# Kernel tuning notes

Hardware: AMD Instinct MI355X
Metric: run time of the kernel (lower is better)

## Reference

```python
import jax, jax.numpy as jnp
import numpy as np

NUM_EDGE_TYPES = 4
TIME_STEPS = (1, 1)  # one propagation step per layer, 2 layers
HIDDEN = 128
N_NODES = 50000
N_EDGES = 400000


def setup_inputs() -> dict:
    key = jax.random.key(0)
    ks = jax.random.split(key, 8)
    states = jax.random.normal(ks[0], (N_NODES, HIDDEN), jnp.float32)
    etype = jax.random.randint(ks[1], (N_EDGES,), 0, NUM_EDGE_TYPES, jnp.int32)
    src = jax.random.randint(ks[2], (N_EDGES,), 0, N_NODES, jnp.int32)
    dst = jax.random.randint(ks[3], (N_EDGES,), 0, N_NODES, jnp.int32)
    edges = jnp.stack([etype, src, dst], axis=-1)  # [E, 3] = (type, src, dst)
    L = len(TIME_STEPS)
    std = HIDDEN ** -0.5  # matches tf.random_normal_initializer(stddev=H**-0.5)
    type_W = jax.random.normal(ks[4], (L, NUM_EDGE_TYPES, HIDDEN, HIDDEN), jnp.float32) * std
    type_b = jax.random.normal(ks[5], (L, NUM_EDGE_TYPES, HIDDEN), jnp.float32) * std
    gru_kernel = jax.random.normal(ks[6], (L, HIDDEN, 3 * HIDDEN), jnp.float32) * std
    gru_rkernel = jax.random.normal(ks[7], (L, HIDDEN, 3 * HIDDEN), jnp.float32) * std
    gru_bias = jnp.zeros((L, 2, 3 * HIDDEN), jnp.float32)  # [input_bias, recurrent_bias]
    return dict(states=states, edges=edges, type_W=type_W, type_b=type_b,
                gru_kernel=gru_kernel, gru_rkernel=gru_rkernel, gru_bias=gru_bias)


def _gru_cell(x, h, kernel, rkernel, bias):
    # tf.keras.layers.GRUCell with defaults (reset_after=True, sigmoid/tanh)
    mx = x @ kernel + bias[0]   # [N, 3H]
    mh = h @ rkernel + bias[1]  # [N, 3H]
    xz, xr, xh = jnp.split(mx, 3, axis=-1)
    hz, hr, hh = jnp.split(mh, 3, axis=-1)
    z = jax.nn.sigmoid(xz + hz)
    r = jax.nn.sigmoid(xr + hr)
    c = jnp.tanh(xh + r * hh)
    return z * h + (1.0 - z) * c


def _propagate(h, layer_no, edges, type_W, type_b):
    etype, src, dst = edges[:, 0], edges[:, 1], edges[:, 2]
    src_states = h[src]  # [E, H] irregular gather
    msgs = jnp.zeros_like(src_states)
    # per-edge-type dense transform, combined via masking (jit-friendly
    # equivalent of tf.dynamic_partition + per-type matmul)
    for t in range(NUM_EDGE_TYPES):
        mt = src_states @ type_W[layer_no, t] + type_b[layer_no, t]
        msgs = msgs + jnp.where((etype == t)[:, None], mt, 0.0)
    # scatter-add messages into destination nodes
    return jax.ops.segment_sum(msgs, dst, num_segments=h.shape[0])


def reference(states, edges, type_W, type_b, gru_kernel, gru_rkernel, gru_bias):
    h = states
    for layer_no, steps in enumerate(TIME_STEPS):
        for _ in range(steps):
            agg = _propagate(h, layer_no, edges, type_W, type_b)
            h = _gru_cell(agg, h, gru_kernel[layer_no], gru_rkernel[layer_no], gru_bias[layer_no])
    return h
```

## Files before the change

### kernel.cpp

```cpp
#include <hip/hip_runtime.h>
#include <hip/hip_bf16.h>

#define H 128
#define NT 4
#define CAP4 40
#define BK 64

typedef __attribute__((ext_vector_type(8))) _Float16 half8;
typedef __attribute__((ext_vector_type(4))) float f32x4;

#if defined(__has_builtin)
#if __has_builtin(__builtin_amdgcn_global_load_lds)
#define HAS_GLL 1
#endif
#endif
#ifndef HAS_GLL
#define HAS_GLL 0
#endif

__device__ __forceinline__ float bf2f(unsigned short u) {
    union { unsigned int i; float f; } v;
    v.i = ((unsigned int)u) << 16;
    return v.f;
}

__device__ __forceinline__ unsigned short f2bf(float f) {
    union { float f; unsigned int i; } v;
    v.f = f;
    unsigned int x = v.i;
    unsigned int r = (x + 0x7fffu + ((x >> 16) & 1u)) >> 16;
    return (unsigned short)r;
}

__device__ __forceinline__ float fsigmoid(float x) {
    return 1.0f / (1.0f + __expf(-x));
}
__device__ __forceinline__ float ftanh(float x) {
    return 1.0f - 2.0f / (__expf(2.0f * x) + 1.0f);
}

__device__ __forceinline__ float readf(const void* p, long i, int isbf) {
    return isbf ? bf2f(((const unsigned short*)p)[i]) : ((const float*)p)[i];
}

__device__ __forceinline__ void gll16(const _Float16* g, _Float16* l) {
#if HAS_GLL
    __builtin_amdgcn_global_load_lds(
        (const __attribute__((address_space(1))) unsigned int*)g,
        (__attribute__((address_space(3))) unsigned int*)l, 16, 0, 0);
#endif
}

__device__ __forceinline__ void stage_tile(
    const _Float16* __restrict__ gbase, int rstride, int row0, int kof,
    int maxrow, _Float16* lds) {
    const int wave = threadIdx.x >> 6, lane = threadIdx.x & 63;
#pragma unroll
    for (int s = 0; s < 4; s++) {
        int R = wave * 32 + s * 8;
        int rl = R + (lane >> 3);
        int rg = row0 + rl;
        if (rg >= maxrow) rg = maxrow - 1;
        int chunk = (lane & 7) ^ (rl & 7);
        const _Float16* gp = gbase + (size_t)rg * rstride + kof + chunk * 8;
#if HAS_GLL
        gll16(gp, lds + R * 64);
#else
        *(half8*)&lds[rl * 64 + (lane & 7) * 8] = *(const half8*)gp;
#endif
    }
}

__device__ __forceinline__ half8 frag(const _Float16* lds, int r, int g) {
    return *(const half8*)&lds[r * 64 + ((g ^ (r & 7)) * 8)];
}

__global__ void detect_dtype(const unsigned short* __restrict__ states_u16,
                             int* __restrict__ flag) {
    __shared__ int cnt;
    if (threadIdx.x == 0) cnt = 0;
    __syncthreads();
    int local = 0;
    for (int i = threadIdx.x; i < 1024; i += 256) {
        unsigned short u = states_u16[2 * i];
        int e = (u >> 7) & 0xFF;
        if (e >= 96 && e <= 158) local++;
    }
    atomicAdd(&cnt, local);
    __syncthreads();
    if (threadIdx.x == 0) *flag = (cnt >= 512) ? 1 : 0;
}

__global__ void prep_all(
    const void* __restrict__ states, const void* __restrict__ type_W,
    const void* __restrict__ type_b, const void* __restrict__ gk,
    const void* __restrict__ gr, const void* __restrict__ grub,
    _Float16* __restrict__ h16, _Float16* __restrict__ BTw,
    _Float16* __restrict__ BTg, float* __restrict__ btab,
    float* __restrict__ gbsum, float* __restrict__ gb0c,
    float* __restrict__ gb1c, int* __restrict__ counts4,
    const int* __restrict__ flag,
    long NNH, int nBTw, int nBTg, int NC4, int LAYERS) {
    long i = (long)blockIdx.x * 256 + threadIdx.x;
    const int fl = *flag;
    if (i < NNH) {
        h16[i] = (_Float16)readf(states, i, fl);
        return;
    }
    i -= NNH;
    if (i < nBTw) {
        int l = (int)(i >> 16);
        int rem = (int)(i & 65535);
        int c = rem >> 9, kk = rem & 511;
        int t = kk >> 7, k = kk & 127;
        BTw[i] = (_Float16)readf(type_W, (((long)(l * NT + t) * H) + k) * H + c, fl);
        return;
    }
    i -= nBTw;
    if (i < nBTg) {
        int l = (int)(i >> 17);
        int rem = (int)(i & 131071);
        int nc = rem >> 8, k = rem & 255;
        int g = nc >> 6, gate = (nc >> 4) & 3, m = nc & 15;
        int c = g * 16 + m;
        float v = 0.0f;
        if (gate == 0) {
            v = (k < 128) ? readf(gk, ((long)l * H + k) * 384 + c, fl)
                          : readf(gr, ((long)l * H + (k - 128)) * 384 + c, fl);
        } else if (gate == 1) {
            v = (k < 128) ? readf(gk, ((long)l * H + k) * 384 + 128 + c, fl)
                          : readf(gr, ((long)l * H + (k - 128)) * 384 + 128 + c, fl);
        } else if (gate == 2) {
            if (k < 128) v = readf(gk, ((long)l * H + k) * 384 + 256 + c, fl);
        } else {
            if (k >= 128) v = readf(gr, ((long)l * H + (k - 128)) * 384 + 256 + c, fl);
        }
        BTg[i] = (_Float16)v;
        return;
    }
    i -= nBTg;
    if (i < NC4) {
        counts4[i] = 0;
        return;
    }
    i -= NC4;
    {
        int j = (int)i;
        if (j < LAYERS * NT * H) btab[j] = readf(type_b, j, fl);
        if (j < LAYERS * 256) {
            int l = j >> 8, c = j & 255;
            gbsum[j] = readf(grub, (long)l * 768 + c, fl) +
                       readf(grub, (long)l * 768 + 384 + c, fl);
        }
        if (j < LAYERS * H) {
            int l = j >> 7, c = j & 127;
            gb0c[j] = readf(grub, (long)l * 768 + 256 + c, fl);
            gb1c[j] = readf(grub, (long)l * 768 + 384 + 256 + c, fl);
        }
    }
}

__global__ void place_edges4(const int* __restrict__ edges, int* __restrict__ counts4,
                             int* __restrict__ buckets4, int NE) {
    int e = blockIdx.x * 256 + threadIdx.x;
    if (e >= NE) return;
    int t = edges[3 * e], src = edges[3 * e + 1], dst = edges[3 * e + 2];
    int slot = atomicAdd(&counts4[dst * 4 + t], 1);
    if (slot < CAP4) buckets4[((size_t)dst * 4 + t) * CAP4 + slot] = src;
}

__global__ __launch_bounds__(256) void gather4(
    const _Float16* __restrict__ h16, const int* __restrict__ counts4,
    const int* __restrict__ buckets4, _Float16* __restrict__ A4, int NN) {
    int node = blockIdx.x * 4 + (threadIdx.x >> 6);
    int lane = threadIdx.x & 63;
    int q = lane >> 4, i = lane & 15;
    if (node >= NN) return;
    int cnt = counts4[node * 4 + q];
    if (cnt > CAP4) cnt = CAP4;
    const int* bkt = buckets4 + ((size_t)node * 4 + q) * CAP4;

    float acc[8] = {};
    int e = 0;
    for (; e + 2 <= cnt; e += 2) {
        int s0 = bkt[e], s1 = bkt[e + 1];
        half8 v0 = *(const half8*)&h16[(size_t)s0 * H + i * 8];
        half8 v1 = *(const half8*)&h16[(size_t)s1 * H + i * 8];
#pragma unroll
        for (int j = 0; j < 8; j++) acc[j] += (float)v0[j] + (float)v1[j];
    }
    if (e < cnt) {
        int s0 = bkt[e];
        half8 v0 = *(const half8*)&h16[(size_t)s0 * H + i * 8];
#pragma unroll
        for (int j = 0; j < 8; j++) acc[j] += (float)v0[j];
    }

    half8 o;
#pragma unroll
    for (int j = 0; j < 8; j++) o[j] = (_Float16)acc[j];
    *(half8*)&A4[((size_t)node * 4 + q) * H + i * 8] = o;
}

__global__ __launch_bounds__(256) void gemm_agg(
    const _Float16* __restrict__ A4,
    const _Float16* __restrict__ BT,
    _Float16* __restrict__ agg,
    const int4* __restrict__ cnt4, const float* __restrict__ btab,
    int Mrows) {
    __shared__ _Float16 As[128 * 64];
    __shared__ _Float16 Bs[128 * 64];

    const int row0 = blockIdx.x * 128;
    const int tid = threadIdx.x;
    const int wave = tid >> 6, lane = tid & 63;
    const int m = lane & 15, quad = lane >> 4;
    const int wr = (wave & 1) * 64, wc = (wave >> 1) * 64;

    f32x4 acc[4][4] = {};

    for (int kc = 0; kc < 8; kc++) {
        const int k0 = kc * BK;
        __syncthreads();
        stage_tile(A4, 512, row0, k0, Mrows, As);
        stage_tile(BT, 512, 0, k0, 128, Bs);
        __syncthreads();

#pragma unroll
        for (int ks = 0; ks < 2; ks++) {
            half8 a[4], b[4];
#pragma unroll
            for (int mt = 0; mt < 4; mt++)
                a[mt] = frag(As, wr + mt * 16 + m, ks * 4 + quad);
#pragma unroll
            for (int nt = 0; nt < 4; nt++)
                b[nt] = frag(Bs, wc + nt * 16 + m, ks * 4 + quad);
#pragma unroll
            for (int mt = 0; mt < 4; mt++)
#pragma unroll
                for (int nt = 0; nt < 4; nt++)
                    acc[mt][nt] = __builtin_amdgcn_mfma_f32_16x16x32_f16(
                        a[mt], b[nt], acc[mt][nt], 0, 0, 0);
        }
    }

#pragma unroll
    for (int mt = 0; mt < 4; mt++) {
#pragma unroll
        for (int i = 0; i < 4; i++) {
            int row = row0 + wr + mt * 16 + quad * 4 + i;
            if (row >= Mrows) continue;
            int4 c4 = cnt4[row];
#pragma unroll
            for (int nt = 0; nt < 4; nt++) {
                int cl = wc + nt * 16 + m;
                float bias = c4.x * btab[cl] + c4.y * btab[128 + cl] +
                             c4.z * btab[256 + cl] + c4.w * btab[384 + cl];
                agg[(size_t)row * H + cl] = (_Float16)(acc[mt][nt][i] + bias);
            }
        }
    }
}

__global__ __launch_bounds__(256) void gru_gemm_gate(
    const _Float16* __restrict__ agg16,
    const _Float16* __restrict__ h16,
    const _Float16* __restrict__ BT,
    const float* __restrict__ gbsum,
    const float* __restrict__ gb0c,
    const float* __restrict__ gb1c,
    _Float16* __restrict__ hnext,
    void* __restrict__ outbuf,
    const int* __restrict__ flag, int rtiles, int NN) {
    __shared__ _Float16 As[128 * 64];
    __shared__ _Float16 Bs[128 * 64];
    __shared__ _Float16 hg[128 * 32];

    const int b = blockIdx.x;
    const int r_lo = b & 7, y = (b >> 3) & 3, macro = b >> 5;
    const int rt = macro * 8 + r_lo;
    if (rt >= rtiles) return;
    const int row0 = rt * 128;
    const int col0 = y * 128;
    const int tid = threadIdx.x;
    const int wave = tid >> 6, lane = tid & 63;
    const int m = lane & 15, quad = lane >> 4;
    const int wr = (wave & 1) * 64, wc = (wave >> 1) * 64;

    f32x4 acc[4][4] = {};

    for (int kc = 0; kc < 4; kc++) {
        const int k0 = kc * BK;
        const int ntA = (kc < 2) ? 2 : 3;
        __syncthreads();
        if (kc < 2) stage_tile(agg16, H, row0, k0, NN, As);
        else        stage_tile(h16, H, row0, k0 - 128, NN, As);
        stage_tile(BT, 256, col0, k0, 512, Bs);
        if (kc == 0) {
#pragma unroll
            for (int s = 0; s < 2; s++) {
                int idx = s * 256 + tid;
                int r = idx >> 2, cseg = (idx & 3) * 8;
                int rg = row0 + r;
                if (rg >= NN) rg = NN - 1;
                *(half8*)&hg[r * 32 + cseg] =
                    *(const half8*)&h16[(size_t)rg * H + y * 32 + cseg];
            }
        }
        __syncthreads();

#pragma unroll
        for (int ks = 0; ks < 2; ks++) {
            half8 a[4], b8[3];
#pragma unroll
            for (int mt = 0; mt < 4; mt++)
                a[mt] = frag(As, wr + mt * 16 + m, ks * 4 + quad);
            b8[0] = frag(Bs, wc + 0 * 16 + m, ks * 4 + quad);
            b8[1] = frag(Bs, wc + 1 * 16 + m, ks * 4 + quad);
            b8[2] = frag(Bs, wc + ntA * 16 + m, ks * 4 + quad);
#pragma unroll
            for (int mt = 0; mt < 4; mt++) {
                acc[mt][0] = __builtin_amdgcn_mfma_f32_16x16x32_f16(
                    a[mt], b8[0], acc[mt][0], 0, 0, 0);
                acc[mt][1] = __builtin_amdgcn_mfma_f32_16x16x32_f16(
                    a[mt], b8[1], acc[mt][1], 0, 0, 0);
                acc[mt][ntA] = __builtin_amdgcn_mfma_f32_16x16x32_f16(
                    a[mt], b8[2], acc[mt][ntA], 0, 0, 0);
            }
        }
    }

    const int g = (col0 + wc) >> 6;
    const int c = g * 16 + m;
    const int chg = (wc >> 2) + m;
    const float bz = gbsum[c];
    const float br = gbsum[128 + c];
    const float bx = gb0c[c];
    const float bh = gb1c[c];
    const int fl = outbuf ? *flag : 0;

#pragma unroll
    for (int mt = 0; mt < 4; mt++) {
#pragma unroll
        for (int i = 0; i < 4; i++) {
            int rl = wr + mt * 16 + quad * 4 + i;
            int row = row0 + rl;
            if (row >= NN) continue;
            float z = fsigmoid(acc[mt][0][i] + bz);
            float r = fsigmoid(acc[mt][1][i] + br);
            float cc = ftanh((acc[mt][2][i] + bx) + r * (acc[mt][3][i] + bh));
            float hv = (float)hg[rl * 32 + chg];
            float hn = z * hv + (1.0f - z) * cc;
            size_t oi = (size_t)row * H + c;
            hnext[oi] = (_Float16)hn;
            if (outbuf) {
                if (fl) ((unsigned short*)outbuf)[oi] = f2bf(hn);
                else    ((float*)outbuf)[oi] = hn;
            }
        }
    }
}

extern "C" void kernel_launch(void* const* d_in, const int* in_sizes, int n_in,
                              void* d_out, int out_size, void* d_ws, size_t ws_size,
                              hipStream_t stream) {
    const void* states = d_in[0];
    const int*  edges  = (const int*)d_in[1];
    const void* type_W = d_in[2];
    const void* type_b = d_in[3];
    const void* gruk   = d_in[4];
    const void* grur   = d_in[5];
    const void* grub   = d_in[6];

    const int NN = in_sizes[0] / H;
    const int NE = in_sizes[1] / 3;
    const int nW = in_sizes[2];
    const int LAYERS = nW / (NT * H * H);

    char* w = (char*)d_ws;
    int* flag = (int*)w;                               w += 64;
    _Float16* h16A  = (_Float16*)w;                    w += (size_t)NN * H * 2;
    _Float16* h16B  = (_Float16*)w;                    w += (size_t)NN * H * 2;
    _Float16* agg16 = (_Float16*)w;                    w += (size_t)NN * H * 2;
    _Float16* A4    = (_Float16*)w;                    w += (size_t)NN * 4 * H * 2;
    _Float16* BTw = (_Float16*)w;                      w += (size_t)LAYERS * H * 512 * 2;
    _Float16* BTg = (_Float16*)w;                      w += (size_t)LAYERS * 512 * 256 * 2;
    float* btab  = (float*)w;                          w += (size_t)LAYERS * NT * H * 4;
    float* gbsum = (float*)w;                          w += (size_t)LAYERS * 256 * 4;
    float* gb0c  = (float*)w;                          w += (size_t)LAYERS * H * 4;
    float* gb1c  = (float*)w;                          w += (size_t)LAYERS * H * 4;
    int* counts4 = (int*)w;                            w += (size_t)NN * 4 * 4;
    int* buckets4 = (int*)w;

    detect_dtype<<<1, 256, 0, stream>>>((const unsigned short*)states, flag);

    const long NNH = (long)NN * H;
    const int nBTw = LAYERS * 65536;
    const int nBTg = LAYERS * 131072;
    const int NC4 = NN * 4;
    const long ptotal = NNH + nBTw + nBTg + NC4 + LAYERS * NT * H;
    prep_all<<<(int)((ptotal + 255) / 256), 256, 0, stream>>>(
        states, type_W, type_b, gruk, grur, grub,
        h16A, BTw, BTg, btab, gbsum, gb0c, gb1c, counts4, flag,
        NNH, nBTw, nBTg, NC4, LAYERS);

    place_edges4<<<(NE + 255) / 256, 256, 0, stream>>>(edges, counts4, buckets4, NE);

    const int rtiles = (NN + 127) / 128;
    const int nb_gru = ((rtiles + 7) / 8) * 32;
    for (int L = 0; L < LAYERS; L++) {
        const _Float16* hcur = (L & 1) ? h16B : h16A;
        _Float16* hnext      = (L & 1) ? h16A : h16B;

        gather4<<<(NN + 3) / 4, 256, 0, stream>>>(hcur, counts4, buckets4, A4, NN);

        gemm_agg<<<rtiles, 256, 0, stream>>>(
            A4, BTw + (size_t)L * H * 512, agg16,
            (const int4*)counts4, btab + (size_t)L * NT * H, NN);

        gru_gemm_gate<<<nb_gru, 256, 0, stream>>>(
            agg16, hcur,
            BTg + (size_t)L * 512 * 256,
            gbsum + (size_t)L * 256, gb0c + (size_t)L * H, gb1c + (size_t)L * H,
            hnext, (L == LAYERS - 1) ? d_out : nullptr, flag, rtiles, NN);
    }
}
```

Before: 291.0 us.

## Fuse edge-type GEMM and GRU GEMM into one kernel with 64-row tiles

Merges the per-type message GEMM and the GRU gate GEMM into a single kernel per layer. The aggregated message tile stays in LDS in swizzled layout instead of being written to and re-read from a global agg buffer, and one kernel launch is removed. Each block now handles 64 rows and loops over all four gate column groups, so the GRU weight tiles are restaged four times per block and the grid shrinks. The previous-state value is now read from global memory inside the gate epilogue rather than from a staged LDS copy.

```diff
diff --git a/kernel.cpp b/kernel.cpp
--- a/kernel.cpp
+++ b/kernel.cpp
@@ -51,13 +51,14 @@
 #endif
 }
 
-__device__ __forceinline__ void stage_tile(
+template<int RPW>
+__device__ __forceinline__ void stage_tileT(
     const _Float16* __restrict__ gbase, int rstride, int row0, int kof,
     int maxrow, _Float16* lds) {
     const int wave = threadIdx.x >> 6, lane = threadIdx.x & 63;
 #pragma unroll
-    for (int s = 0; s < 4; s++) {
-        int R = wave * 32 + s * 8;
+    for (int s = 0; s < RPW / 8; s++) {
+        int R = wave * RPW + s * 8;
         int rl = R + (lane >> 3);
         int rg = row0 + rl;
         if (rg >= maxrow) rg = maxrow - 1;
@@ -202,160 +203,137 @@
     *(half8*)&A4[((size_t)node * 4 + q) * H + i * 8] = o;
 }
 
-__global__ __launch_bounds__(256) void gemm_agg(
+__global__ __launch_bounds__(256, 4) void layer_fused(
     const _Float16* __restrict__ A4,
-    const _Float16* __restrict__ BT,
-    _Float16* __restrict__ agg,
-    const int4* __restrict__ cnt4, const float* __restrict__ btab,
-    int Mrows) {
-    __shared__ _Float16 As[128 * 64];
-    __shared__ _Float16 Bs[128 * 64];
-
-    const int row0 = blockIdx.x * 128;
-    const int tid = threadIdx.x;
-    const int wave = tid >> 6, lane = tid & 63;
-    const int m = lane & 15, quad = lane >> 4;
-    const int wr = (wave & 1) * 64, wc = (wave >> 1) * 64;
-
-    f32x4 acc[4][4] = {};
-
-    for (int kc = 0; kc < 8; kc++) {
-        const int k0 = kc * BK;
-        __syncthreads();
-        stage_tile(A4, 512, row0, k0, Mrows, As);
-        stage_tile(BT, 512, 0, k0, 128, Bs);
-        __syncthreads();
-
-#pragma unroll
-        for (int ks = 0; ks < 2; ks++) {
-            half8 a[4], b[4];
-#pragma unroll
-            for (int mt = 0; mt < 4; mt++)
-                a[mt] = frag(As, wr + mt * 16 + m, ks * 4 + quad);
-#pragma unroll
-            for (int nt = 0; nt < 4; nt++)
-                b[nt] = frag(Bs, wc + nt * 16 + m, ks * 4 + quad);
-#pragma unroll
-            for (int mt = 0; mt < 4; mt++)
-#pragma unroll
-                for (int nt = 0; nt < 4; nt++)
-                    acc[mt][nt] = __builtin_amdgcn_mfma_f32_16x16x32_f16(
-                        a[mt], b[nt], acc[mt][nt], 0, 0, 0);
-        }
-    }
-
-#pragma unroll
-    for (int mt = 0; mt < 4; mt++) {
-#pragma unroll
-        for (int i = 0; i < 4; i++) {
-            int row = row0 + wr + mt * 16 + quad * 4 + i;
-            if (row >= Mrows) continue;
-            int4 c4 = cnt4[row];
-#pragma unroll
-            for (int nt = 0; nt < 4; nt++) {
-                int cl = wc + nt * 16 + m;
-                float bias = c4.x * btab[cl] + c4.y * btab[128 + cl] +
-                             c4.z * btab[256 + cl] + c4.w * btab[384 + cl];
-                agg[(size_t)row * H + cl] = (_Float16)(acc[mt][nt][i] + bias);
-            }
-        }
-    }
-}
-
-__global__ __launch_bounds__(256) void gru_gemm_gate(
-    const _Float16* __restrict__ agg16,
     const _Float16* __restrict__ h16,
-    const _Float16* __restrict__ BT,
+    const _Float16* __restrict__ BTw,
+    const _Float16* __restrict__ BTg,
+    const float* __restrict__ btab,
+    const int4* __restrict__ cnt4,
     const float* __restrict__ gbsum,
     const float* __restrict__ gb0c,
     const float* __restrict__ gb1c,
     _Float16* __restrict__ hnext,
     void* __restrict__ outbuf,
-    const int* __restrict__ flag, int rtiles, int NN) {
-    __shared__ _Float16 As[128 * 64];
-    __shared__ _Float16 Bs[128 * 64];
-    __shared__ _Float16 hg[128 * 32];
-
-    const int b = blockIdx.x;
-    const int r_lo = b & 7, y = (b >> 3) & 3, macro = b >> 5;
-    const int rt = macro * 8 + r_lo;
-    if (rt >= rtiles) return;
-    const int row0 = rt * 128;
-    const int col0 = y * 128;
+    const int* __restrict__ flag, int NN) {
+    __shared__ _Float16 scratch[12288];
+    __shared__ _Float16 aggL[8192];
+
+    const int row0 = blockIdx.x * 64;
     const int tid = threadIdx.x;
     const int wave = tid >> 6, lane = tid & 63;
     const int m = lane & 15, quad = lane >> 4;
-    const int wr = (wave & 1) * 64, wc = (wave >> 1) * 64;
-
-    f32x4 acc[4][4] = {};
-
-    for (int kc = 0; kc < 4; kc++) {
+    const int wr = (wave & 1) * 32, wc = (wave >> 1) * 64;
+
+    f32x4 acc[2][4] = {};
+
+    for (int kc = 0; kc < 8; kc++) {
         const int k0 = kc * BK;
-        const int ntA = (kc < 2) ? 2 : 3;
         __syncthreads();
-        if (kc < 2) stage_tile(agg16, H, row0, k0, NN, As);
-        else        stage_tile(h16, H, row0, k0 - 128, NN, As);
-        stage_tile(BT, 256, col0, k0, 512, Bs);
-        if (kc == 0) {
-#pragma unroll
-            for (int s = 0; s < 2; s++) {
-                int idx = s * 256 + tid;
-                int r = idx >> 2, cseg = (idx & 3) * 8;
-                int rg = row0 + r;
-                if (rg >= NN) rg = NN - 1;
-                *(half8*)&hg[r * 32 + cseg] =
-                    *(const half8*)&h16[(size_t)rg * H + y * 32 + cseg];
-            }
-        }
+        stage_tileT<16>(A4, 512, row0, k0, NN, scratch);
+        stage_tileT<32>(BTw, 512, 0, k0, 128, scratch + 4096);
         __syncthreads();
-
 #pragma unroll
         for (int ks = 0; ks < 2; ks++) {
-            half8 a[4], b8[3];
-#pragma unroll
-            for (int mt = 0; mt < 4; mt++)
-                a[mt] = frag(As, wr + mt * 16 + m, ks * 4 + quad);
-            b8[0] = frag(Bs, wc + 0 * 16 + m, ks * 4 + quad);
-            b8[1] = frag(Bs, wc + 1 * 16 + m, ks * 4 + quad);
-            b8[2] = frag(Bs, wc + ntA * 16 + m, ks * 4 + quad);
-#pragma unroll
-            for (int mt = 0; mt < 4; mt++) {
-                acc[mt][0] = __builtin_amdgcn_mfma_f32_16x16x32_f16(
-                    a[mt], b8[0], acc[mt][0], 0, 0, 0);
-                acc[mt][1] = __builtin_amdgcn_mfma_f32_16x16x32_f16(
-                    a[mt], b8[1], acc[mt][1], 0, 0, 0);
-                acc[mt][ntA] = __builtin_amdgcn_mfma_f32_16x16x32_f16(
-                    a[mt], b8[2], acc[mt][ntA], 0, 0, 0);
-            }
-        }
-    }
-
-    const int g = (col0 + wc) >> 6;
-    const int c = g * 16 + m;
-    const int chg = (wc >> 2) + m;
-    const float bz = gbsum[c];
-    const float br = gbsum[128 + c];
-    const float bx = gb0c[c];
-    const float bh = gb1c[c];
-    const int fl = outbuf ? *flag : 0;
-
-#pragma unroll
-    for (int mt = 0; mt < 4; mt++) {
+            half8 a[2], b[4];
+#pragma unroll
+            for (int mt = 0; mt < 2; mt++)
+                a[mt] = frag(scratch, wr + mt * 16 + m, ks * 4 + quad);
+#pragma unroll
+            for (int nt = 0; nt < 4; nt++)
+                b[nt] = frag(scratch + 4096, wc + nt * 16 + m, ks * 4 + quad);
+#pragma unroll
+            for (int mt = 0; mt < 2; mt++)
+#pragma unroll
+                for (int nt = 0; nt < 4; nt++)
+                    acc[mt][nt] = __builtin_amdgcn_mfma_f32_16x16x32_f16(
+                        a[mt], b[nt], acc[mt][nt], 0, 0, 0);
+        }
+    }
+
+#pragma unroll
+    for (int mt = 0; mt < 2; mt++) {
 #pragma unroll
         for (int i = 0; i < 4; i++) {
             int rl = wr + mt * 16 + quad * 4 + i;
-            int row = row0 + rl;
-            if (row >= NN) continue;
-            float z = fsigmoid(acc[mt][0][i] + bz);
-            float r = fsigmoid(acc[mt][1][i] + br);
-            float cc = ftanh((acc[mt][2][i] + bx) + r * (acc[mt][3][i] + bh));
-            float hv = (float)hg[rl * 32 + chg];
-            float hn = z * hv + (1.0f - z) * cc;
-            size_t oi = (size_t)row * H + c;
-            hnext[oi] = (_Float16)hn;
-            if (outbuf) {
-                if (fl) ((unsigned short*)outbuf)[oi] = f2bf(hn);
-                else    ((float*)outbuf)[oi] = hn;
+            int rg = row0 + rl;
+            if (rg >= NN) rg = NN - 1;
+            int4 c4 = cnt4[rg];
+#pragma unroll
+            for (int nt = 0; nt < 4; nt++) {
+                int c = wc + nt * 16 + m;
+                float bias = c4.x * btab[c] + c4.y * btab[128 + c] +
+                             c4.z * btab[256 + c] + c4.w * btab[384 + c];
+                int tile = c >> 6, cc = c & 63, g = cc >> 3;
+                aggL[tile * 4096 + rl * 64 + ((g ^ (rl & 7)) * 8) + (cc & 7)] =
+                    (_Float16)(acc[mt][nt][i] + bias);
+            }
+        }
+    }
+
+    const int fl = outbuf ? *flag : 0;
+    for (int y = 0; y < 4; y++) {
+#pragma unroll
+        for (int mt = 0; mt < 2; mt++)
+#pragma unroll
+            for (int nt = 0; nt < 4; nt++)
+                acc[mt][nt] = (f32x4){0.f, 0.f, 0.f, 0.f};
+
+        for (int kc = 0; kc < 4; kc++) {
+            const int ntA = (kc < 2) ? 2 : 3;
+            __syncthreads();
+            stage_tileT<32>(BTg, 256, y * 128, kc * BK, 512, scratch);
+            if (kc >= 2)
+                stage_tileT<16>(h16, H, row0, (kc - 2) * BK, NN, scratch + 8192);
+            __syncthreads();
+#pragma unroll
+            for (int ks = 0; ks < 2; ks++) {
+                const _Float16* Asrc =
+                    (kc < 2) ? (aggL + kc * 4096) : (scratch + 8192);
+                half8 a[2], b3[3];
+#pragma unroll
+                for (int mt = 0; mt < 2; mt++)
+                    a[mt] = frag(Asrc, wr + mt * 16 + m, ks * 4 + quad);
+                b3[0] = frag(scratch, wc + 0 * 16 + m, ks * 4 + quad);
+                b3[1] = frag(scratch, wc + 1 * 16 + m, ks * 4 + quad);
+                b3[2] = frag(scratch, wc + ntA * 16 + m, ks * 4 + quad);
+#pragma unroll
+                for (int mt = 0; mt < 2; mt++) {
+                    acc[mt][0] = __builtin_amdgcn_mfma_f32_16x16x32_f16(
+                        a[mt], b3[0], acc[mt][0], 0, 0, 0);
+                    acc[mt][1] = __builtin_amdgcn_mfma_f32_16x16x32_f16(
+                        a[mt], b3[1], acc[mt][1], 0, 0, 0);
+                    acc[mt][ntA] = __builtin_amdgcn_mfma_f32_16x16x32_f16(
+                        a[mt], b3[2], acc[mt][ntA], 0, 0, 0);
+                }
+            }
+        }
+
+        const int g8 = y * 2 + (wc >> 6);
+        const int c = g8 * 16 + m;
+        const float bz = gbsum[c];
+        const float br = gbsum[128 + c];
+        const float bx = gb0c[c];
+        const float bh = gb1c[c];
+#pragma unroll
+        for (int mt = 0; mt < 2; mt++) {
+#pragma unroll
+            for (int i = 0; i < 4; i++) {
+                int rl = wr + mt * 16 + quad * 4 + i;
+                int row = row0 + rl;
+                if (row >= NN) continue;
+                float z = fsigmoid(acc[mt][0][i] + bz);
+                float r = fsigmoid(acc[mt][1][i] + br);
+                float ccand =
+                    ftanh((acc[mt][2][i] + bx) + r * (acc[mt][3][i] + bh));
+                float hv = (float)h16[(size_t)row * H + c];
+                float hn = z * hv + (1.0f - z) * ccand;
+                size_t oi = (size_t)row * H + c;
+                hnext[oi] = (_Float16)hn;
+                if (outbuf) {
+                    if (fl) ((unsigned short*)outbuf)[oi] = f2bf(hn);
+                    else    ((float*)outbuf)[oi] = hn;
+                }
             }
         }
     }
@@ -381,7 +359,6 @@
     int* flag = (int*)w;                               w += 64;
     _Float16* h16A  = (_Float16*)w;                    w += (size_t)NN * H * 2;
     _Float16* h16B  = (_Float16*)w;                    w += (size_t)NN * H * 2;
-    _Float16* agg16 = (_Float16*)w;                    w += (size_t)NN * H * 2;
     _Float16* A4    = (_Float16*)w;                    w += (size_t)NN * 4 * H * 2;
     _Float16* BTw = (_Float16*)w;                      w += (size_t)LAYERS * H * 512 * 2;
     _Float16* BTg = (_Float16*)w;                      w += (size_t)LAYERS * 512 * 256 * 2;
@@ -406,22 +383,19 @@
 
     place_edges4<<<(NE + 255) / 256, 256, 0, stream>>>(edges, counts4, buckets4, NE);
 
-    const int rtiles = (NN + 127) / 128;
-    const int nb_gru = ((rtiles + 7) / 8) * 32;
+    const int rt64 = (NN + 63) / 64;
     for (int L = 0; L < LAYERS; L++) {
         const _Float16* hcur = (L & 1) ? h16B : h16A;
         _Float16* hnext      = (L & 1) ? h16A : h16B;
 
         gather4<<<(NN + 3) / 4, 256, 0, stream>>>(hcur, counts4, buckets4, A4, NN);
 
-        gemm_agg<<<rtiles, 256, 0, stream>>>(
-            A4, BTw + (size_t)L * H * 512, agg16,
-            (const int4*)counts4, btab + (size_t)L * NT * H, NN);
-
-        gru_gemm_gate<<<nb_gru, 256, 0, stream>>>(
-            agg16, hcur,
+        layer_fused<<<rt64, 256, 0, stream>>>(
+            A4, hcur,
+            BTw + (size_t)L * H * 512,
             BTg + (size_t)L * 512 * 256,
+            btab + (size_t)L * NT * H, (const int4*)counts4,
             gbsum + (size_t)L * 256, gb0c + (size_t)L * H, gb1c + (size_t)L * H,
-            hnext, (L == LAYERS - 1) ? d_out : nullptr, flag, rtiles, NN);
-    }
-}
+            hnext, (L == LAYERS - 1) ? d_out : nullptr, flag, NN);
+    }
+}
```

After: 277.7 us. -4.6%, faster.
